# Performance work log

Hardware: AMD Instinct MI355X
Metric: run time of the kernel (lower is better)

## Reference

```python
import jax, jax.numpy as jnp
import numpy as np

C = 128          # hidden_channels
H = 8            # num_heads
D = C // H       # head dim = 16
OUT = 64         # out_channels
L = 2            # num_layers
NN = (30000, 60000, 6000)                 # poi, road, region node counts
NE = (200000, 300000, 200000, 100000)     # edges per edge type
ETS = ((0, 1), (1, 1), (1, 2), (2, 0))    # (src_type, dst_type) per edge type


def setup_inputs():
    key = jax.random.key(0)
    ks = iter(jax.random.split(key, 40))
    s = 1.0 / np.sqrt(C)
    sd = 1.0 / np.sqrt(D)
    inp = {}
    inp['x_poi'] = jax.random.normal(next(ks), (NN[0], C), jnp.float32)
    inp['x_road'] = jax.random.normal(next(ks), (NN[1], C), jnp.float32)
    inp['x_region'] = jax.random.normal(next(ks), (NN[2], C), jnp.float32)
    for et, (si, di) in enumerate(ETS):
        inp[f'e{et}_src'] = jax.random.randint(next(ks), (NE[et],), 0, NN[si], jnp.int32)
        inp[f'e{et}_dst'] = jax.random.randint(next(ks), (NE[et],), 0, NN[di], jnp.int32)
    # per-node-type input projection
    inp['lin_w'] = jax.random.normal(next(ks), (3, C, C), jnp.float32) * s
    inp['lin_b'] = jax.random.normal(next(ks), (3, C), jnp.float32) * 0.01
    # per-layer, per-node-type K/Q/V and output projections
    for nm in ('kw', 'qw', 'vw', 'aw'):
        inp[nm] = jax.random.normal(next(ks), (L, 3, C, C), jnp.float32) * s
    for nm in ('kb', 'qb', 'vb', 'ab'):
        inp[nm] = jax.random.normal(next(ks), (L, 3, C), jnp.float32) * 0.01
    # per-layer, per-edge-type relation matrices and priors
    inp['a_rel'] = jax.random.normal(next(ks), (L, 4, H, D, D), jnp.float32) * sd
    inp['m_rel'] = jax.random.normal(next(ks), (L, 4, H, D, D), jnp.float32) * sd
    inp['p_rel'] = jnp.ones((L, 4, H), jnp.float32)
    inp['skip'] = jnp.ones((L, 3), jnp.float32)
    inp['out_w'] = jax.random.normal(next(ks), (C, OUT), jnp.float32) * s
    inp['out_b'] = jnp.zeros((OUT,), jnp.float32)
    return inp


def _seg_softmax(alpha, dst, n):
    amax = jax.lax.stop_gradient(jax.ops.segment_max(alpha, dst, num_segments=n))
    ex = jnp.exp(alpha - amax[dst])
    den = jax.ops.segment_sum(ex, dst, num_segments=n)
    return ex / (den[dst] + 1e-16)


def _hgt_forward(xs, edges, lin_w, lin_b, kw, kb, qw, qb, vw, vb, aw, ab,
                 a_rel, m_rel, p_rel, skip, out_w, out_b):
    # per-node-type input linear + relu
    xs = [jax.nn.relu(xs[i] @ lin_w[i] + lin_b[i]) for i in range(3)]
    scale = 1.0 / np.sqrt(D)
    for l in range(L):
        k = [(xs[i] @ kw[l, i] + kb[l, i]).reshape(-1, H, D) for i in range(3)]
        q = [(xs[i] @ qw[l, i] + qb[l, i]).reshape(-1, H, D) for i in range(3)]
        v = [(xs[i] @ vw[l, i] + vb[l, i]).reshape(-1, H, D) for i in range(3)]
        agg = [jnp.zeros((NN[i], H, D), xs[i].dtype) for i in range(3)]
        for et, (si, di) in enumerate(ETS):
            src, dst = edges[et]
            n = NN[di]
            ke = jnp.einsum('ehd,hdf->ehf', k[si][src], a_rel[l, et])   # [E,H,D]
            alpha = jnp.einsum('ehd,ehd->eh', q[di][dst], ke) * p_rel[l, et] * scale
            alpha = _seg_softmax(alpha, dst, n)                          # [E,H]
            m = jnp.einsum('ehd,hdf->ehf', v[si][src], m_rel[l, et])    # [E,H,D]
            agg[di] = agg[di] + jax.ops.segment_sum(m * alpha[..., None], dst, num_segments=n)
        new_xs = []
        for i in range(3):
            o = jax.nn.gelu(agg[i].reshape(-1, C)) @ aw[l, i] + ab[l, i]
            beta = jax.nn.sigmoid(skip[l, i])
            o = beta * o + (1.0 - beta) * xs[i]
            new_xs.append(jax.nn.relu(o))  # HGT applies activation after each conv
        xs = new_xs
    return (xs[0] @ out_w + out_b, xs[1] @ out_w + out_b, xs[2] @ out_w + out_b)


def reference(x_poi, x_road, x_region,
              e0_src, e0_dst, e1_src, e1_dst, e2_src, e2_dst, e3_src, e3_dst,
              lin_w, lin_b, kw, kb, qw, qb, vw, vb, aw, ab,
              a_rel, m_rel, p_rel, skip, out_w, out_b):
    edges = ((e0_src, e0_dst), (e1_src, e1_dst), (e2_src, e2_dst), (e3_src, e3_dst))
    return _hgt_forward([x_poi, x_road, x_region], edges,
                        lin_w, lin_b, kw, kb, qw, qb, vw, vb, aw, ab,
                        a_rel, m_rel, p_rel, skip, out_w, out_b)
```

## Files before the change

### kernel.cpp

```cpp
#include <hip/hip_runtime.h>
#include <cstddef>
#include <cstdint>


typedef __attribute__((ext_vector_type(8))) short short8;
typedef __attribute__((ext_vector_type(4))) float floatx4;

__device__ __forceinline__ float gelu_fast(float x) {
    float u = 1.5957691216057308f * x * (1.0f + 0.044715f * x * x);
    return x / (1.0f + __expf(-u));
}

__device__ __forceinline__ unsigned short f2bf(float f) {
    unsigned u = __float_as_uint(f);
    u += 0x7fffu + ((u >> 16) & 1);
    return (unsigned short)(u >> 16);
}

__device__ __forceinline__ float bf2f(unsigned short h) {
    return __uint_as_float((unsigned)h << 16);
}

__device__ __forceinline__ void up8(uint4 u, float* f) {
    f[0] = __uint_as_float(u.x << 16); f[1] = __uint_as_float(u.x & 0xffff0000u);
    f[2] = __uint_as_float(u.y << 16); f[3] = __uint_as_float(u.y & 0xffff0000u);
    f[4] = __uint_as_float(u.z << 16); f[5] = __uint_as_float(u.z & 0xffff0000u);
    f[6] = __uint_as_float(u.w << 16); f[7] = __uint_as_float(u.w & 0xffff0000u);
}

__device__ __forceinline__ uint4 pk8(const float* f) {
    uint4 u;
    u.x = (unsigned)f2bf(f[0]) | ((unsigned)f2bf(f[1]) << 16);
    u.y = (unsigned)f2bf(f[2]) | ((unsigned)f2bf(f[3]) << 16);
    u.z = (unsigned)f2bf(f[4]) | ((unsigned)f2bf(f[5]) << 16);
    u.w = (unsigned)f2bf(f[6]) | ((unsigned)f2bf(f[7]) << 16);
    return u;
}

__global__ __launch_bounds__(256, 2) void gemm_proj_all(
    const unsigned short* __restrict__ xs_bf,
    const unsigned short* __restrict__ Wl,
    const float* __restrict__ bl,
    unsigned short* __restrict__ proj)
{
    const int    NN_[3]  = {30000, 60000, 6000};
    const int    NPAN[3] = {469, 938, 94};
    const int    OFFr[3] = {0, 30000, 90000};
    const int    WOFF[3] = {0, 49152, 131072};
    const int    BOFF[3] = {0, 384, 1024};
    const size_t POFF[3] = {0, 11520000u, 49920000u};
    const int    LDO[3]  = {384, 640, 384};

    int b = blockIdx.x, t, cp, rb;
    if (b < 590)      { t = 1; cp = b / 118; rb = b - cp * 118; }
    else if (b < 767) { int lb = b - 590; t = 0; cp = lb / 59; rb = lb - cp * 59; }
    else              { int lb = b - 767; t = 2; cp = lb / 12; rb = lb - cp * 12; }
    int p0 = rb * 8, p1 = p0 + 8;
    if (p1 > NPAN[t]) p1 = NPAN[t];

    const unsigned short* Abf = xs_bf + (size_t)OFFr[t] * 128;
    const unsigned short* Wt  = Wl + WOFF[t];
    const float* bias = bl + BOFF[t] + cp * 128;
    unsigned short* outbf = proj + POFF[t];
    const int ldo = LDO[t], Nrows = NN_[t];

    const int wave = threadIdx.x >> 6, lane = threadIdx.x & 63;
    const int quad = lane >> 4, l16 = lane & 15;

    short8 B[2][4][4];
    {
        const unsigned short* wb = Wt + (size_t)(cp * 128 + l16) * 128 + quad * 8;
        #pragma unroll
        for (int T = 0; T < 2; ++T)
            #pragma unroll
            for (int c = 0; c < 4; ++c)
                #pragma unroll
                for (int kc = 0; kc < 4; ++kc)
                    B[T][c][kc] = *(const short8*)(wb + (size_t)(T * 64 + c * 16) * 128 + kc * 32);
    }
    float4 bv[2][4];
    #pragma unroll
    for (int T = 0; T < 2; ++T)
        #pragma unroll
        for (int c = 0; c < 4; ++c)
            bv[T][c] = *(const float4*)(bias + T * 64 + c * 16 + quad * 4);

    short8 Acur[4];
    {
        int m = p0 * 64 + wave * 16 + l16; if (m >= Nrows) m = Nrows - 1;
        const unsigned short* ap = Abf + (size_t)m * 128 + quad * 8;
        #pragma unroll
        for (int kc = 0; kc < 4; ++kc) Acur[kc] = *(const short8*)(ap + kc * 32);
    }
    for (int p = p0; p < p1; ++p) {
        short8 Anx[4];
        {
            int m = (p + 1) * 64 + wave * 16 + l16; if (m >= Nrows) m = Nrows - 1;
            const unsigned short* ap = Abf + (size_t)m * 128 + quad * 8;
            #pragma unroll
            for (int kc = 0; kc < 4; ++kc) Anx[kc] = *(const short8*)(ap + kc * 32);
        }
        floatx4 acc[2][4];
        #pragma unroll
        for (int T = 0; T < 2; ++T)
            #pragma unroll
            for (int c = 0; c < 4; ++c) acc[T][c] = (floatx4){0.f, 0.f, 0.f, 0.f};
        #pragma unroll
        for (int kc = 0; kc < 4; ++kc)
            #pragma unroll
            for (int T = 0; T < 2; ++T)
                #pragma unroll
                for (int c = 0; c < 4; ++c)
                    acc[T][c] = __builtin_amdgcn_mfma_f32_16x16x32_bf16(B[T][c][kc], Acur[kc], acc[T][c], 0, 0, 0);
        int node = p * 64 + wave * 16 + l16;
        if (node < Nrows) {
            unsigned short* op = outbf + (size_t)node * ldo + cp * 128 + quad * 4;
            #pragma unroll
            for (int T = 0; T < 2; ++T)
                #pragma unroll
                for (int c = 0; c < 4; ++c) {
                    uint2 u;
                    u.x = (unsigned)f2bf(acc[T][c][0] + bv[T][c].x) |
                          ((unsigned)f2bf(acc[T][c][1] + bv[T][c].y) << 16);
                    u.y = (unsigned)f2bf(acc[T][c][2] + bv[T][c].z) |
                          ((unsigned)f2bf(acc[T][c][3] + bv[T][c].w) << 16);
                    *(uint2*)(op + T * 64 + c * 16) = u;
                }
        }
        #pragma unroll
        for (int kc = 0; kc < 4; ++kc) Acur[kc] = Anx[kc];
    }
}

template<bool AF32, bool GIN, bool SKIP>
__global__ __launch_bounds__(256, 2) void gemm_node(
    const void* __restrict__ a0v, const void* __restrict__ a1v, const void* __restrict__ a2v,
    const unsigned short* __restrict__ WtB, const float* __restrict__ biasB,
    const unsigned short* __restrict__ xoldB, const float* __restrict__ skipB,
    unsigned short* __restrict__ outB)
{
    const int TN[3]   = {30000, 60000, 6000};
    const int NPAN[3] = {469, 938, 94};
    const int TOFF[3] = {0, 30000, 90000};
    int b = blockIdx.x, t, rb;
    if (b < 118)      { t = 0; rb = b; }
    else if (b < 353) { t = 1; rb = b - 118; }
    else              { t = 2; rb = b - 353; }
    int p0 = rb * 4, p1 = p0 + 4;
    if (p1 > NPAN[t]) p1 = NPAN[t];
    int Nrows = TN[t];
    const void* av = (t == 0) ? a0v : (t == 1) ? a1v : a2v;
    const unsigned short* xold = xoldB + (size_t)TOFF[t] * 128;
    unsigned short* out = outB + (size_t)TOFF[t] * 128;

    const int wave = threadIdx.x >> 6, lane = threadIdx.x & 63;
    const int quad = lane >> 4, l16 = lane & 15;

    short8 B[8][4];
    {
        const unsigned short* wb = WtB + (size_t)t * 16384 + (size_t)l16 * 128 + quad * 8;
        #pragma unroll
        for (int c = 0; c < 8; ++c)
            #pragma unroll
            for (int kc = 0; kc < 4; ++kc)
                B[c][kc] = *(const short8*)(wb + (size_t)c * 2048 + kc * 32);
    }
    float beta = 0.f, omb = 0.f;
    if (SKIP) { beta = 1.0f / (1.0f + __expf(-skipB[t])); omb = 1.0f - beta; }

    short8 Acur[4];
    {
        int m = p0 * 64 + wave * 16 + l16; if (m >= Nrows) m = Nrows - 1;
        size_t base = (size_t)m * 128 + quad * 8;
        #pragma unroll
        for (int kc = 0; kc < 4; ++kc) {
            if (AF32) {
                const float* ap = (const float*)av + base;
                float4 f0 = *(const float4*)(ap + kc * 32);
                float4 f1 = *(const float4*)(ap + kc * 32 + 4);
                float af[8] = {f0.x, f0.y, f0.z, f0.w, f1.x, f1.y, f1.z, f1.w};
                short8 a;
                #pragma unroll
                for (int i = 0; i < 8; ++i) a[i] = (short)f2bf(af[i]);
                Acur[kc] = a;
            } else if (GIN) {
                const unsigned short* ap = (const unsigned short*)av + base;
                short8 a8 = *(const short8*)(ap + kc * 32);
                short8 a;
                #pragma unroll
                for (int i = 0; i < 8; ++i)
                    a[i] = (short)f2bf(gelu_fast(bf2f((unsigned short)a8[i])));
                Acur[kc] = a;
            } else {
                const unsigned short* ap = (const unsigned short*)av + base;
                Acur[kc] = *(const short8*)(ap + kc * 32);
            }
        }
    }
    for (int p = p0; p < p1; ++p) {
        float4 Fnx[4][2];
        short8 Snx[4];
        {
            int m = (p + 1) * 64 + wave * 16 + l16; if (m >= Nrows) m = Nrows - 1;
            size_t base = (size_t)m * 128 + quad * 8;
            #pragma unroll
            for (int kc = 0; kc < 4; ++kc) {
                if (AF32) {
                    const float* ap = (const float*)av + base;
                    Fnx[kc][0] = *(const float4*)(ap + kc * 32);
                    Fnx[kc][1] = *(const float4*)(ap + kc * 32 + 4);
                } else {
                    const unsigned short* ap = (const unsigned short*)av + base;
                    Snx[kc] = *(const short8*)(ap + kc * 32);
                }
            }
        }
        int node = p * 64 + wave * 16 + l16;
        int ncl = (node < Nrows) ? node : (Nrows - 1);
        uint2 xo[8];
        if (SKIP) {
            #pragma unroll
            for (int c = 0; c < 8; ++c)
                xo[c] = *(const uint2*)(xold + (size_t)ncl * 128 + c * 16 + quad * 4);
        }
        floatx4 acc[8];
        #pragma unroll
        for (int c = 0; c < 8; ++c) acc[c] = (floatx4){0.f, 0.f, 0.f, 0.f};
        #pragma unroll
        for (int kc = 0; kc < 4; ++kc)
            #pragma unroll
            for (int c = 0; c < 8; ++c)
                acc[c] = __builtin_amdgcn_mfma_f32_16x16x32_bf16(B[c][kc], Acur[kc], acc[c], 0, 0, 0);
        if (node < Nrows) {
            #pragma unroll
            for (int c = 0; c < 8; ++c) {
                int col0 = c * 16 + quad * 4;
                float4 bv = *(const float4*)(biasB + t * 128 + col0);
                float o0 = acc[c][0] + bv.x, o1 = acc[c][1] + bv.y;
                float o2 = acc[c][2] + bv.z, o3 = acc[c][3] + bv.w;
                if (SKIP) {
                    o0 = beta * o0 + omb * __uint_as_float(xo[c].x << 16);
                    o1 = beta * o1 + omb * __uint_as_float(xo[c].x & 0xffff0000u);
                    o2 = beta * o2 + omb * __uint_as_float(xo[c].y << 16);
                    o3 = beta * o3 + omb * __uint_as_float(xo[c].y & 0xffff0000u);
                }
                o0 = fmaxf(o0, 0.f); o1 = fmaxf(o1, 0.f);
                o2 = fmaxf(o2, 0.f); o3 = fmaxf(o3, 0.f);
                uint2 u;
                u.x = (unsigned)f2bf(o0) | ((unsigned)f2bf(o1) << 16);
                u.y = (unsigned)f2bf(o2) | ((unsigned)f2bf(o3) << 16);
                *(uint2*)(out + (size_t)node * 128 + col0) = u;
            }
        }
        #pragma unroll
        for (int kc = 0; kc < 4; ++kc) {
            if (AF32) {
                float af[8] = {Fnx[kc][0].x, Fnx[kc][0].y, Fnx[kc][0].z, Fnx[kc][0].w,
                               Fnx[kc][1].x, Fnx[kc][1].y, Fnx[kc][1].z, Fnx[kc][1].w};
                short8 a;
                #pragma unroll
                for (int i = 0; i < 8; ++i) a[i] = (short)f2bf(af[i]);
                Acur[kc] = a;
            } else if (GIN) {
                short8 a;
                #pragma unroll
                for (int i = 0; i < 8; ++i)
                    a[i] = (short)f2bf(gelu_fast(bf2f((unsigned short)Snx[kc][i])));
                Acur[kc] = a;
            } else {
                Acur[kc] = Snx[kc];
            }
        }
    }
}

__global__ __launch_bounds__(256, 3) void gemm_out(
    const unsigned short* __restrict__ Abf,
    const unsigned short* __restrict__ Wt,
    const float* __restrict__ bias,
    float* __restrict__ out, int Nrows)
{
    const int wave = threadIdx.x >> 6, lane = threadIdx.x & 63;
    const int quad = lane >> 4, l16 = lane & 15;
    int p0 = blockIdx.x * 4, p1 = p0 + 4;

    short8 B[4][4];
    {
        const unsigned short* wb = Wt + (size_t)l16 * 128 + quad * 8;
        #pragma unroll
        for (int c = 0; c < 4; ++c)
            #pragma unroll
            for (int kc = 0; kc < 4; ++kc)
                B[c][kc] = *(const short8*)(wb + (size_t)c * 2048 + kc * 32);
    }
    float4 bv[4];
    #pragma unroll
    for (int c = 0; c < 4; ++c) bv[c] = *(const float4*)(bias + c * 16 + quad * 4);

    short8 Acur[4];
    {
        int m = p0 * 64 + wave * 16 + l16; if (m >= Nrows) m = Nrows - 1;
        const unsigned short* ap = Abf + (size_t)m * 128 + quad * 8;
        #pragma unroll
        for (int kc = 0; kc < 4; ++kc) Acur[kc] = *(const short8*)(ap + kc * 32);
    }
    for (int p = p0; p < p1; ++p) {
        short8 Anx[4];
        {
            int m = (p + 1) * 64 + wave * 16 + l16; if (m >= Nrows) m = Nrows - 1;
            const unsigned short* ap = Abf + (size_t)m * 128 + quad * 8;
            #pragma unroll
            for (int kc = 0; kc < 4; ++kc) Anx[kc] = *(const short8*)(ap + kc * 32);
        }
        floatx4 acc[4];
        #pragma unroll
        for (int c = 0; c < 4; ++c) acc[c] = (floatx4){0.f, 0.f, 0.f, 0.f};
        #pragma unroll
        for (int kc = 0; kc < 4; ++kc)
            #pragma unroll
            for (int c = 0; c < 4; ++c)
                acc[c] = __builtin_amdgcn_mfma_f32_16x16x32_bf16(B[c][kc], Acur[kc], acc[c], 0, 0, 0);
        int node = p * 64 + wave * 16 + l16;
        if (node < Nrows) {
            #pragma unroll
            for (int c = 0; c < 4; ++c) {
                float4 o;
                o.x = acc[c][0] + bv[c].x; o.y = acc[c][1] + bv[c].y;
                o.z = acc[c][2] + bv[c].z; o.w = acc[c][3] + bv[c].w;
                *(float4*)(out + (size_t)node * 64 + c * 16 + quad * 4) = o;
            }
        }
        #pragma unroll
        for (int kc = 0; kc < 4; ++kc) Acur[kc] = Anx[kc];
    }
}

__global__ __launch_bounds__(128) void prep_all(
    const float* __restrict__ qw, const float* __restrict__ qb,
    const float* __restrict__ kw, const float* __restrict__ kb,
    const float* __restrict__ vw, const float* __restrict__ vb,
    const float* __restrict__ a_rel, const float* __restrict__ m_rel,
    const float* __restrict__ lin_w, const float* __restrict__ aw,
    const float* __restrict__ ow,
    unsigned short* __restrict__ Wpack, float* __restrict__ bpack,
    unsigned short* __restrict__ lwt, unsigned short* __restrict__ awt,
    unsigned short* __restrict__ owt)
{
    const int pre[3] = {0, 49152, 131072};
    const int preB[3] = {0, 384, 1024};
    int b = blockIdx.x;
    if (b < 768) {
        int n = threadIdx.x;
        int k = b & 127, r = b >> 7, t = r % 3, l = r / 3;
        unsigned short* Wp = Wpack + (size_t)l * 180224 + pre[t];
        Wp[(size_t)n * 128 + k] = f2bf(qw[(size_t)(l * 3 + t) * 16384 + (size_t)k * 128 + n]);
        if (k == 0) bpack[l * 1408 + preB[t] + n] = qb[(l * 3 + t) * 128 + n];
    } else if (b < 1792) {
        const int SIv[4] = {0, 1, 1, 2};
        const int SLOT[4] = {0, 0, 1, 0};
        int bb = b - 768;
        int hf = threadIdx.x, h = hf >> 4, f = hf & 15;
        int c = bb & 127, et = (bb >> 7) & 3, l = bb >> 9;
        int si = SIv[et];
        const float* kwp  = kw + (size_t)(l * 3 + si) * 16384;
        const float* vwp  = vw + (size_t)(l * 3 + si) * 16384;
        const float* kbp  = kb + (size_t)(l * 3 + si) * 128;
        const float* vbp  = vb + (size_t)(l * 3 + si) * 128;
        const float* arel = a_rel + (size_t)(l * 4 + et) * 2048;
        const float* mrel = m_rel + (size_t)(l * 4 + et) * 2048;
        float sk = 0.f, sv = 0.f;
        #pragma unroll
        for (int d = 0; d < 16; ++d) {
            float ar = arel[(h * 16 + d) * 16 + f];
            float mr = mrel[(h * 16 + d) * 16 + f];
            sk = fmaf(kwp[c * 128 + h * 16 + d], ar, sk);
            sv = fmaf(vwp[c * 128 + h * 16 + d], mr, sv);
        }
        int rowoff = 128 + 256 * SLOT[et];
        unsigned short* Wp = Wpack + (size_t)l * 180224 + pre[si];
        Wp[(size_t)(rowoff + hf) * 128 + c]       = f2bf(sk);
        Wp[(size_t)(rowoff + 128 + hf) * 128 + c] = f2bf(sv);
        if (c == 0) {
            float bk = 0.f, bvv = 0.f;
            #pragma unroll
            for (int d = 0; d < 16; ++d) {
                bk  = fmaf(kbp[h * 16 + d], arel[(h * 16 + d) * 16 + f], bk);
                bvv = fmaf(vbp[h * 16 + d], mrel[(h * 16 + d) * 16 + f], bvv);
            }
            float* bp = bpack + l * 1408 + preB[si];
            bp[rowoff + hf]       = bk;
            bp[rowoff + 128 + hf] = bvv;
        }
    } else if (b < 2944) {
        int bb = b - 1792;
        int n = threadIdx.x, k = bb & 127, mi = bb >> 7;
        const float* w; unsigned short* wt; int m;
        if (mi < 3) { w = lin_w; wt = lwt; m = mi; }
        else        { w = aw;    wt = awt; m = mi - 3; }
        wt[(size_t)m * 16384 + (size_t)n * 128 + k] =
            f2bf(w[(size_t)m * 16384 + (size_t)k * 128 + n]);
    } else {
        int k = b - 2944, n = threadIdx.x;
        if (n < 64) owt[(size_t)n * 128 + k] = f2bf(ow[(size_t)k * 64 + n]);
    }
}

__global__ __launch_bounds__(256) void hist_all(
    const int* __restrict__ d0, const int* __restrict__ d1,
    const int* __restrict__ d2, const int* __restrict__ d3,
    int* __restrict__ deg4)
{
    const int Ev[4] = {200000, 300000, 200000, 100000};
    int et = blockIdx.y;
    int e = blockIdx.x * 256 + threadIdx.x;
    if (e >= Ev[et]) return;
    const int* d = et == 0 ? d0 : et == 1 ? d1 : et == 2 ? d2 : d3;
    atomicAdd(&deg4[et * 60000 + d[e]], 1);
}

__global__ __launch_bounds__(256) void scan_tile_all(
    int* __restrict__ deg4,
    int* __restrict__ r0, int* __restrict__ r1, int* __restrict__ r2, int* __restrict__ r3,
    int* __restrict__ tsum4)
{
    const int Ndv[4] = {60000, 60000, 6000, 30000};
    __shared__ int ls[256];
    int et = blockIdx.y;
    int n = Ndv[et];
    int* deg = deg4 + et * 60000;
    int* rowptr = et == 0 ? r0 : et == 1 ? r1 : et == 2 ? r2 : r3;
    int b = blockIdx.x, tid = threadIdx.x;
    int base = b * 1024 + tid * 4;
    int v0 = 0, v1 = 0, v2 = 0, v3 = 0;
    if (base + 3 < n) {
        int4 t = *(const int4*)(deg + base);
        v0 = t.x; v1 = t.y; v2 = t.z; v3 = t.w;
        *(int4*)(deg + base) = make_int4(0, 0, 0, 0);
    } else {
        if (base + 0 < n) { v0 = deg[base + 0]; deg[base + 0] = 0; }
        if (base + 1 < n) { v1 = deg[base + 1]; deg[base + 1] = 0; }
        if (base + 2 < n) { v2 = deg[base + 2]; deg[base + 2] = 0; }
        if (base + 3 < n) { v3 = deg[base + 3]; deg[base + 3] = 0; }
    }
    int s = v0 + v1 + v2 + v3;
    ls[tid] = s;
    __syncthreads();
    #pragma unroll
    for (int off = 1; off < 256; off <<= 1) {
        int t = (tid >= off) ? ls[tid - off] : 0;
        __syncthreads();
        ls[tid] += t;
        __syncthreads();
    }
    int run = ls[tid] - s;
    int o0 = run; run += v0;
    int o1 = run; run += v1;
    int o2 = run; run += v2;
    int o3 = run;
    if (base + 3 < n) {
        *(int4*)(rowptr + base) = make_int4(o0, o1, o2, o3);
    } else {
        if (base + 0 < n) rowptr[base + 0] = o0;
        if (base + 1 < n) rowptr[base + 1] = o1;
        if (base + 2 < n) rowptr[base + 2] = o2;
    }
    if (tid == 255) tsum4[et * 64 + b] = ls[255];
}

__global__ __launch_bounds__(256) void scan_add_all(
    int* __restrict__ r0, int* __restrict__ r1, int* __restrict__ r2, int* __restrict__ r3,
    const int* __restrict__ tsum4)
{
    const int Ndv[4] = {60000, 60000, 6000, 30000};
    __shared__ int ts[64];
    int et = blockIdx.y;
    int n = Ndv[et];
    int* rowptr = et == 0 ? r0 : et == 1 ? r1 : et == 2 ? r2 : r3;
    int tid = threadIdx.x;
    if (tid < 64) ts[tid] = tsum4[et * 64 + tid];
    __syncthreads();
    int i = blockIdx.x * 256 + tid;
    int tile = i >> 10;
    int pre = 0;
    for (int j = 0; j < tile; ++j) pre += ts[j];
    if (i < n) rowptr[i] += pre;
    if (blockIdx.x == 0 && tid == 0) {
        int nt = (n + 1023) >> 10, tot = 0;
        for (int j = 0; j < nt; ++j) tot += ts[j];
        rowptr[n] = tot;
    }
}

__global__ __launch_bounds__(256) void fill_all(
    const int* __restrict__ s0, const int* __restrict__ d0,
    const int* __restrict__ s1, const int* __restrict__ d1,
    const int* __restrict__ s2, const int* __restrict__ d2,
    const int* __restrict__ s3, const int* __restrict__ d3,
    const int* __restrict__ r0, const int* __restrict__ r1,
    const int* __restrict__ r2, const int* __restrict__ r3,
    int* __restrict__ deg4,
    int* __restrict__ c0, int* __restrict__ c1, int* __restrict__ c2, int* __restrict__ c3)
{
    const int Ev[4] = {200000, 300000, 200000, 100000};
    int et = blockIdx.y;
    int e = blockIdx.x * 256 + threadIdx.x;
    if (e >= Ev[et]) return;
    const int* src = et == 0 ? s0 : et == 1 ? s1 : et == 2 ? s2 : s3;
    const int* dst = et == 0 ? d0 : et == 1 ? d1 : et == 2 ? d2 : d3;
    const int* rowptr = et == 0 ? r0 : et == 1 ? r1 : et == 2 ? r2 : r3;
    int* csr = et == 0 ? c0 : et == 1 ? c1 : et == 2 ? c2 : c3;
    int d = dst[e];
    int pos = atomicAdd(&deg4[et * 60000 + d], 1);
    csr[rowptr[d] + pos] = src[e];
}

__device__ __forceinline__ void attn_edge(
    uint4 k0, uint4 k1, uint4 v0, uint4 v1,
    const float* qf, float ph, float& m, float& l, float* o)
{
    float kf[16];
    up8(k0, kf); up8(k1, kf + 8);
    float a = 0.f;
    #pragma unroll
    for (int i = 0; i < 16; ++i) a = fmaf(qf[i], kf[i], a);
    a *= ph;
    float d = a - m;
    if (d > 8.f) {
        float sc = __expf(-d);
        l *= sc;
        #pragma unroll
        for (int i = 0; i < 16; ++i) o[i] *= sc;
        m = a; d = 0.f;
    }
    float w = __expf(d);
    l += w;
    float vf[16];
    up8(v0, vf); up8(v1, vf + 8);
    #pragma unroll
    for (int i = 0; i < 16; ++i) o[i] = fmaf(w, vf[i], o[i]);
}

__device__ __forceinline__ void attn_run(
    const int* __restrict__ csr, int beg, int end,
    const unsigned short* __restrict__ kbase, int ld,
    const float* qf, float ph, float& m, float& l, float* o)
{
    int n = end - beg;
    if (n <= 0) return;
    const uint4* pA = (const uint4*)(kbase + (size_t)csr[beg] * ld);
    uint4 A0 = pA[0], A1 = pA[1], A2 = pA[16], A3 = pA[17];
    uint4 B0 = A0, B1 = A1, B2 = A2, B3 = A3;
    if (n > 1) {
        const uint4* pB = (const uint4*)(kbase + (size_t)csr[beg + 1] * ld);
        B0 = pB[0]; B1 = pB[1]; B2 = pB[16]; B3 = pB[17];
    }
    int j = beg;
    for (; j + 3 < end; j += 2) {
        const uint4* pC = (const uint4*)(kbase + (size_t)csr[j + 2] * ld);
        const uint4* pD = (const uint4*)(kbase + (size_t)csr[j + 3] * ld);
        uint4 C0 = pC[0], C1 = pC[1], C2 = pC[16], C3 = pC[17];
        uint4 D0 = pD[0], D1 = pD[1], D2 = pD[16], D3 = pD[17];
        float kf0[16], kf1[16];
        up8(A0, kf0); up8(A1, kf0 + 8);
        up8(B0, kf1); up8(B1, kf1 + 8);
        float a0 = 0.f, a1 = 0.f;
        #pragma unroll
        for (int i = 0; i < 16; ++i) {
            a0 = fmaf(qf[i], kf0[i], a0);
            a1 = fmaf(qf[i], kf1[i], a1);
        }
        a0 *= ph; a1 *= ph;
        float hi = fmaxf(a0, a1);
        float d = hi - m;
        if (d > 8.f) {
            float sc = __expf(-d);
            l *= sc;
            #pragma unroll
            for (int i = 0; i < 16; ++i) o[i] *= sc;
            m = hi;
        }
        float w0 = __expf(a0 - m), w1 = __expf(a1 - m);
        l += w0 + w1;
        float vf0[16], vf1[16];
        up8(A2, vf0); up8(A3, vf0 + 8);
        up8(B2, vf1); up8(B3, vf1 + 8);
        #pragma unroll
        for (int i = 0; i < 16; ++i)
            o[i] = fmaf(w1, vf1[i], fmaf(w0, vf0[i], o[i]));
        A0 = C0; A1 = C1; A2 = C2; A3 = C3;
        B0 = D0; B1 = D1; B2 = D2; B3 = D3;
    }
    int rem = end - j;
    attn_edge(A0, A1, A2, A3, qf, ph, m, l, o);
    if (rem >= 2) attn_edge(B0, B1, B2, B3, qf, ph, m, l, o);
    if (rem == 3) {
        const uint4* pC = (const uint4*)(kbase + (size_t)csr[j + 2] * ld);
        attn_edge(pC[0], pC[1], pC[16], pC[17], qf, ph, m, l, o);
    }
}

__device__ __forceinline__ void merge_sm(float& m, float& l, float* o, int st)
{
    float mp = __shfl_xor(m, st);
    float lp = __shfl_xor(l, st);
    float mn = fmaxf(m, mp);
    float sc  = (l  > 0.f) ? __expf(m  - mn) : 0.f;
    float scp = (lp > 0.f) ? __expf(mp - mn) : 0.f;
    l = l * sc + lp * scp;
    #pragma unroll
    for (int i = 0; i < 16; ++i) {
        float op = __shfl_xor(o[i], st);
        o[i] = o[i] * sc + op * scp;
    }
    m = mn;
}

__global__ __launch_bounds__(256) void agg_all(
    const int* __restrict__ rp0, const int* __restrict__ cs0,
    const int* __restrict__ rp1, const int* __restrict__ cs1,
    const int* __restrict__ rp2, const int* __restrict__ cs2,
    const int* __restrict__ rp3, const int* __restrict__ cs3,
    const unsigned short* __restrict__ P0, const unsigned short* __restrict__ P1,
    const unsigned short* __restrict__ P2,
    const float* __restrict__ prl,
    unsigned short* __restrict__ num)
{
    int gb = blockIdx.x, tid = threadIdx.x;
    float qf[16], o[16], r[16];
    if (gb < 3750) {
        int t = gb * 256 + tid;
        int node = t >> 4, h = t & 7, half = (t >> 3) & 1;
        const uint4* qp = (const uint4*)(P1 + (size_t)node * 640 + h * 16);
        up8(qp[0], qf); up8(qp[1], qf + 8);
        const int* csr = half ? cs1 : cs0;
        const int* rp  = half ? rp1 : rp0;
        const unsigned short* kb = half ? (P1 + 128 + h * 16) : (P0 + 128 + h * 16);
        int ld = half ? 640 : 384;
        float ph = prl[(half ? 8 : 0) + h] * 0.25f;
        float m = -INFINITY, l = 0.f;
        #pragma unroll
        for (int i = 0; i < 16; ++i) o[i] = 0.f;
        attn_run(csr, rp[node], rp[node + 1], kb, ld, qf, ph, m, l, o);
        float inv = 1.f / (l + 1e-16f);
        #pragma unroll
        for (int i = 0; i < 16; ++i) r[i] = inv * o[i];
        #pragma unroll
        for (int i = 0; i < 16; ++i) r[i] += __shfl_xor(r[i], 8);
        if (half) return;
        uint4* np = (uint4*)(num + (size_t)(30000 + node) * 128 + h * 16);
        np[0] = pk8(r); np[1] = pk8(r + 8);
    } else if (gb < 4500) {
        int t = (gb - 3750) * 256 + tid;
        int node = t >> 5, h = t & 7, sub = (t >> 3) & 3;
        int beg0 = rp2[node], end0 = rp2[node + 1];
        int n = end0 - beg0;
        int beg = beg0 + ((n * sub) >> 2);
        int end = beg0 + ((n * (sub + 1)) >> 2);
        const uint4* qp = (const uint4*)(P2 + (size_t)node * 384 + h * 16);
        up8(qp[0], qf); up8(qp[1], qf + 8);
        float m = -INFINITY, l = 0.f;
        #pragma unroll
        for (int i = 0; i < 16; ++i) o[i] = 0.f;
        attn_run(cs2, beg, end, P1 + 384 + h * 16, 640,
                 qf, prl[16 + h] * 0.25f, m, l, o);
        merge_sm(m, l, o, 8);
        merge_sm(m, l, o, 16);
        if (sub) return;
        float inv = 1.f / (l + 1e-16f);
        #pragma unroll
        for (int i = 0; i < 16; ++i) r[i] = inv * o[i];
        uint4* np = (uint4*)(num + (size_t)(90000 + node) * 128 + h * 16);
        np[0] = pk8(r); np[1] = pk8(r + 8);
    } else {
        int t = (gb - 4500) * 256 + tid;
        if (t >= 240000) return;
        int node = t >> 3, h = t & 7;
        const uint4* qp = (const uint4*)(P0 + (size_t)node * 384 + h * 16);
        up8(qp[0], qf); up8(qp[1], qf + 8);
        float m = -INFINITY, l = 0.f;
        #pragma unroll
        for (int i = 0; i < 16; ++i) o[i] = 0.f;
        attn_run(cs3, rp3[node], rp3[node + 1], P2 + 128 + h * 16, 384,
                 qf, prl[24 + h] * 0.25f, m, l, o);
        float inv = 1.f / (l + 1e-16f);
        #pragma unroll
        for (int i = 0; i < 16; ++i) r[i] = inv * o[i];
        uint4* np = (uint4*)(num + (size_t)node * 128 + h * 16);
        np[0] = pk8(r); np[1] = pk8(r + 8);
    }
}

extern "C" void kernel_launch(void* const* d_in, const int* in_sizes, int n_in,
                              void* d_out, int out_size, void* d_ws, size_t ws_size,
                              hipStream_t stream)
{
    (void)in_sizes; (void)n_in; (void)out_size; (void)ws_size;

    const float* xin[3] = {(const float*)d_in[0], (const float*)d_in[1], (const float*)d_in[2]};
    const int* esrc[4] = {(const int*)d_in[3], (const int*)d_in[5], (const int*)d_in[7], (const int*)d_in[9]};
    const int* edst[4] = {(const int*)d_in[4], (const int*)d_in[6], (const int*)d_in[8], (const int*)d_in[10]};
    const float* lin_w = (const float*)d_in[11];
    const float* lin_b = (const float*)d_in[12];
    const float* kw = (const float*)d_in[13];
    const float* qw = (const float*)d_in[14];
    const float* vw = (const float*)d_in[15];
    const float* aw = (const float*)d_in[16];
    const float* kb = (const float*)d_in[17];
    const float* qb = (const float*)d_in[18];
    const float* vb = (const float*)d_in[19];
    const float* ab = (const float*)d_in[20];
    const float* a_rel = (const float*)d_in[21];
    const float* m_rel = (const float*)d_in[22];
    const float* p_rel = (const float*)d_in[23];
    const float* skip  = (const float*)d_in[24];
    const float* out_w = (const float*)d_in[25];
    const float* out_b = (const float*)d_in[26];

    float* ws = (float*)d_ws;
    unsigned short* num   = (unsigned short*)ws;
    unsigned short* xs_bf = (unsigned short*)(ws + 6144000);
    unsigned short* proj  = (unsigned short*)(ws + 12288000);
    unsigned short* Wpack = (unsigned short*)(ws + 38400000);
    unsigned short* lwt   = (unsigned short*)(ws + 38580224);
    unsigned short* awt   = (unsigned short*)(ws + 38604800);
    unsigned short* owt   = (unsigned short*)(ws + 38653952);
    float*          bpack = ws + 38658048;
    int*            deg4  = (int*)(ws + 38660864);
    int*            tsum4 = (int*)(ws + 38900864);
    int* rp[4];
    rp[0] = (int*)(ws + 38901120);
    rp[1] = (int*)(ws + 38961128);
    rp[2] = (int*)(ws + 39021136);
    rp[3] = (int*)(ws + 39027144);
    int* cs[4];
    cs[0] = (int*)(ws + 39057152);
    cs[1] = (int*)(ws + 39257152);
    cs[2] = (int*)(ws + 39557152);
    cs[3] = (int*)(ws + 39757152);

    unsigned short* P[3];
    P[0] = proj;
    P[1] = proj + (size_t)30000 * 384;
    P[2] = proj + (size_t)30000 * 384 + (size_t)60000 * 640;

    dim3 blk(256);

    hipMemsetAsync(deg4, 0, 960000, stream);
    hist_all<<<dim3(1172, 4), blk, 0, stream>>>(edst[0], edst[1], edst[2], edst[3], deg4);
    scan_tile_all<<<dim3(59, 4), blk, 0, stream>>>(deg4, rp[0], rp[1], rp[2], rp[3], tsum4);
    scan_add_all<<<dim3(235, 4), blk, 0, stream>>>(rp[0], rp[1], rp[2], rp[3], tsum4);
    fill_all<<<dim3(1172, 4), blk, 0, stream>>>(
        esrc[0], edst[0], esrc[1], edst[1], esrc[2], edst[2], esrc[3], edst[3],
        rp[0], rp[1], rp[2], rp[3], deg4, cs[0], cs[1], cs[2], cs[3]);

    prep_all<<<dim3(3072), dim3(128), 0, stream>>>(
        qw, qb, kw, kb, vw, vb, a_rel, m_rel, lin_w, aw, out_w,
        Wpack, bpack, lwt, awt, owt);

    gemm_node<true, false, false><<<dim3(377), blk, 0, stream>>>(
        xin[0], xin[1], xin[2], lwt, lin_b, nullptr, nullptr, xs_bf);

    for (int l = 0; l < 2; ++l) {
        gemm_proj_all<<<dim3(803), blk, 0, stream>>>(
            xs_bf, Wpack + (size_t)l * 180224, bpack + l * 1408, proj);

        agg_all<<<dim3(5438), blk, 0, stream>>>(
            rp[0], cs[0], rp[1], cs[1], rp[2], cs[2], rp[3], cs[3],
            P[0], P[1], P[2], p_rel + (size_t)l * 32, num);

        gemm_node<false, true, true><<<dim3(377), blk, 0, stream>>>(
            num, num + (size_t)30000 * 128, num + (size_t)90000 * 128,
            awt + (size_t)l * 3 * 16384, ab + (size_t)l * 3 * 128,
            xs_bf, skip + l * 3, xs_bf);
    }

    gemm_out<<<dim3(375), blk, 0, stream>>>(
        xs_bf, owt, out_b, (float*)d_out, 96000);
}
```

Before: 567.5 us.

## Fuse histogram with weight prep and CSR fill with input projection GEMM

Merges the degree-histogram kernel with the weight-packing prep kernel into one launch, and merges the CSR fill kernel with the input-projection GEMM, dispatching by block index. This cuts two kernel launches and lets the independent graph-building and dense work run concurrently on different blocks. The new input GEMM computes all 128 output columns per wave with 4 panels per block and a ReLU epilogue. It adds register pressure, through launch_bounds(256,2) and 32 B fragments held per lane, and mixes heterogeneous blocks in one grid.

Measured after the change: 555.2 us. 1.02x faster.

```diff
diff --git a/kernel.cpp b/kernel.cpp
--- a/kernel.cpp
+++ b/kernel.cpp
@@ -335,7 +335,10 @@
     }
 }
 
-__global__ __launch_bounds__(128) void prep_all(
+__global__ __launch_bounds__(256) void hist_prep(
+    const int* __restrict__ d0, const int* __restrict__ d1,
+    const int* __restrict__ d2, const int* __restrict__ d3,
+    int* __restrict__ deg4,
     const float* __restrict__ qw, const float* __restrict__ qb,
     const float* __restrict__ kw, const float* __restrict__ kb,
     const float* __restrict__ vw, const float* __restrict__ vb,
@@ -346,20 +349,31 @@
     unsigned short* __restrict__ lwt, unsigned short* __restrict__ awt,
     unsigned short* __restrict__ owt)
 {
+    int b = blockIdx.x;
+    if (b < 4688) {
+        const int Ev[4] = {200000, 300000, 200000, 100000};
+        int et = b / 1172, bx = b - et * 1172;
+        int e = bx * 256 + threadIdx.x;
+        if (e >= Ev[et]) return;
+        const int* d = et == 0 ? d0 : et == 1 ? d1 : et == 2 ? d2 : d3;
+        atomicAdd(&deg4[et * 60000 + d[e]], 1);
+        return;
+    }
     const int pre[3] = {0, 49152, 131072};
     const int preB[3] = {0, 384, 1024};
-    int b = blockIdx.x;
-    if (b < 768) {
-        int n = threadIdx.x;
-        int k = b & 127, r = b >> 7, t = r % 3, l = r / 3;
+    int unit = (b - 4688) * 2 + (threadIdx.x >> 7);
+    int tid = threadIdx.x & 127;
+    if (unit < 768) {
+        int n = tid;
+        int k = unit & 127, r = unit >> 7, t = r % 3, l = r / 3;
         unsigned short* Wp = Wpack + (size_t)l * 180224 + pre[t];
         Wp[(size_t)n * 128 + k] = f2bf(qw[(size_t)(l * 3 + t) * 16384 + (size_t)k * 128 + n]);
         if (k == 0) bpack[l * 1408 + preB[t] + n] = qb[(l * 3 + t) * 128 + n];
-    } else if (b < 1792) {
+    } else if (unit < 1792) {
         const int SIv[4] = {0, 1, 1, 2};
         const int SLOT[4] = {0, 0, 1, 0};
-        int bb = b - 768;
-        int hf = threadIdx.x, h = hf >> 4, f = hf & 15;
+        int bb = unit - 768;
+        int hf = tid, h = hf >> 4, f = hf & 15;
         int c = bb & 127, et = (bb >> 7) & 3, l = bb >> 9;
         int si = SIv[et];
         const float* kwp  = kw + (size_t)(l * 3 + si) * 16384;
@@ -391,31 +405,18 @@
             bp[rowoff + hf]       = bk;
             bp[rowoff + 128 + hf] = bvv;
         }
-    } else if (b < 2944) {
-        int bb = b - 1792;
-        int n = threadIdx.x, k = bb & 127, mi = bb >> 7;
+    } else if (unit < 2944) {
+        int bb = unit - 1792;
+        int n = tid, k = bb & 127, mi = bb >> 7;
         const float* w; unsigned short* wt; int m;
         if (mi < 3) { w = lin_w; wt = lwt; m = mi; }
         else        { w = aw;    wt = awt; m = mi - 3; }
         wt[(size_t)m * 16384 + (size_t)n * 128 + k] =
             f2bf(w[(size_t)m * 16384 + (size_t)k * 128 + n]);
     } else {
-        int k = b - 2944, n = threadIdx.x;
+        int k = unit - 2944, n = tid;
         if (n < 64) owt[(size_t)n * 128 + k] = f2bf(ow[(size_t)k * 64 + n]);
     }
-}
-
-__global__ __launch_bounds__(256) void hist_all(
-    const int* __restrict__ d0, const int* __restrict__ d1,
-    const int* __restrict__ d2, const int* __restrict__ d3,
-    int* __restrict__ deg4)
-{
-    const int Ev[4] = {200000, 300000, 200000, 100000};
-    int et = blockIdx.y;
-    int e = blockIdx.x * 256 + threadIdx.x;
-    if (e >= Ev[et]) return;
-    const int* d = et == 0 ? d0 : et == 1 ? d1 : et == 2 ? d2 : d3;
-    atomicAdd(&deg4[et * 60000 + d[e]], 1);
 }
 
 __global__ __launch_bounds__(256) void scan_tile_all(
@@ -491,7 +492,7 @@
     }
 }
 
-__global__ __launch_bounds__(256) void fill_all(
+__global__ __launch_bounds__(256, 2) void fill_nodein(
     const int* __restrict__ s0, const int* __restrict__ d0,
     const int* __restrict__ s1, const int* __restrict__ d1,
     const int* __restrict__ s2, const int* __restrict__ d2,
@@ -499,19 +500,114 @@
     const int* __restrict__ r0, const int* __restrict__ r1,
     const int* __restrict__ r2, const int* __restrict__ r3,
     int* __restrict__ deg4,
-    int* __restrict__ c0, int* __restrict__ c1, int* __restrict__ c2, int* __restrict__ c3)
-{
-    const int Ev[4] = {200000, 300000, 200000, 100000};
-    int et = blockIdx.y;
-    int e = blockIdx.x * 256 + threadIdx.x;
-    if (e >= Ev[et]) return;
-    const int* src = et == 0 ? s0 : et == 1 ? s1 : et == 2 ? s2 : s3;
-    const int* dst = et == 0 ? d0 : et == 1 ? d1 : et == 2 ? d2 : d3;
-    const int* rowptr = et == 0 ? r0 : et == 1 ? r1 : et == 2 ? r2 : r3;
-    int* csr = et == 0 ? c0 : et == 1 ? c1 : et == 2 ? c2 : c3;
-    int d = dst[e];
-    int pos = atomicAdd(&deg4[et * 60000 + d], 1);
-    csr[rowptr[d] + pos] = src[e];
+    int* __restrict__ c0, int* __restrict__ c1, int* __restrict__ c2, int* __restrict__ c3,
+    const float* __restrict__ x0, const float* __restrict__ x1,
+    const float* __restrict__ x2,
+    const unsigned short* __restrict__ lwt, const float* __restrict__ lin_b,
+    unsigned short* __restrict__ xs_bf)
+{
+    int b = blockIdx.x;
+    if (b < 4688) {
+        const int Ev[4] = {200000, 300000, 200000, 100000};
+        int et = b / 1172, bx = b - et * 1172;
+        int e = bx * 256 + threadIdx.x;
+        if (e >= Ev[et]) return;
+        const int* src = et == 0 ? s0 : et == 1 ? s1 : et == 2 ? s2 : s3;
+        const int* dst = et == 0 ? d0 : et == 1 ? d1 : et == 2 ? d2 : d3;
+        const int* rowptr = et == 0 ? r0 : et == 1 ? r1 : et == 2 ? r2 : r3;
+        int* csr = et == 0 ? c0 : et == 1 ? c1 : et == 2 ? c2 : c3;
+        int dd = dst[e];
+        int pos = atomicAdd(&deg4[et * 60000 + dd], 1);
+        csr[rowptr[dd] + pos] = src[e];
+        return;
+    }
+    const int TN[3]   = {30000, 60000, 6000};
+    const int NPAN[3] = {469, 938, 94};
+    const int TOFF[3] = {0, 30000, 90000};
+    int nb = b - 4688, t, rb;
+    if (nb < 118)      { t = 0; rb = nb; }
+    else if (nb < 353) { t = 1; rb = nb - 118; }
+    else               { t = 2; rb = nb - 353; }
+    int p0 = rb * 4, p1 = p0 + 4;
+    if (p1 > NPAN[t]) p1 = NPAN[t];
+    int Nrows = TN[t];
+    const float* av = (t == 0) ? x0 : (t == 1) ? x1 : x2;
+    unsigned short* out = xs_bf + (size_t)TOFF[t] * 128;
+
+    const int wave = threadIdx.x >> 6, lane = threadIdx.x & 63;
+    const int quad = lane >> 4, l16 = lane & 15;
+
+    short8 B[8][4];
+    {
+        const unsigned short* wb = lwt + (size_t)t * 16384 + (size_t)l16 * 128 + quad * 8;
+        #pragma unroll
+        for (int c = 0; c < 8; ++c)
+            #pragma unroll
+            for (int kc = 0; kc < 4; ++kc)
+                B[c][kc] = *(const short8*)(wb + (size_t)c * 2048 + kc * 32);
+    }
+    short8 Acur[4];
+    {
+        int m = p0 * 64 + wave * 16 + l16; if (m >= Nrows) m = Nrows - 1;
+        size_t base = (size_t)m * 128 + quad * 8;
+        #pragma unroll
+        for (int kc = 0; kc < 4; ++kc) {
+            const float* ap = av + base;
+            float4 f0 = *(const float4*)(ap + kc * 32);
+            float4 f1 = *(const float4*)(ap + kc * 32 + 4);
+            float af[8] = {f0.x, f0.y, f0.z, f0.w, f1.x, f1.y, f1.z, f1.w};
+            short8 a;
+            #pragma unroll
+            for (int i = 0; i < 8; ++i) a[i] = (short)f2bf(af[i]);
+            Acur[kc] = a;
+        }
+    }
+    for (int p = p0; p < p1; ++p) {
+        float4 Fnx[4][2];
+        {
+            int m = (p + 1) * 64 + wave * 16 + l16; if (m >= Nrows) m = Nrows - 1;
+            size_t base = (size_t)m * 128 + quad * 8;
+            #pragma unroll
+            for (int kc = 0; kc < 4; ++kc) {
+                const float* ap = av + base;
+                Fnx[kc][0] = *(const float4*)(ap + kc * 32);
+                Fnx[kc][1] = *(const float4*)(ap + kc * 32 + 4);
+            }
+        }
+        floatx4 acc[8];
+        #pragma unroll
+        for (int c = 0; c < 8; ++c) acc[c] = (floatx4){0.f, 0.f, 0.f, 0.f};
+        #pragma unroll
+        for (int kc = 0; kc < 4; ++kc)
+            #pragma unroll
+            for (int c = 0; c < 8; ++c)
+                acc[c] = __builtin_amdgcn_mfma_f32_16x16x32_bf16(B[c][kc], Acur[kc], acc[c], 0, 0, 0);
+        int node = p * 64 + wave * 16 + l16;
+        if (node < Nrows) {
+            #pragma unroll
+            for (int c = 0; c < 8; ++c) {
+                int col0 = c * 16 + quad * 4;
+                float4 bv = *(const float4*)(lin_b + t * 128 + col0);
+                float o0 = fmaxf(acc[c][0] + bv.x, 0.f);
+                float o1 = fmaxf(acc[c][1] + bv.y, 0.f);
+                float o2 = fmaxf(acc[c][2] + bv.z, 0.f);
+                float o3 = fmaxf(acc[c][3] + bv.w, 0.f);
+                uint2 u;
+                u.x = (unsigned)f2bf(o0) | ((unsigned)f2bf(o1) << 16);
+                u.y = (unsigned)f2bf(o2) | ((unsigned)f2bf(o3) << 16);
+                *(uint2*)(out + (size_t)node * 128 + col0) = u;
+            }
+        }
+        #pragma unroll
+        for (int kc = 0; kc < 4; ++kc) {
+            float af[8] = {Fnx[kc][0].x, Fnx[kc][0].y, Fnx[kc][0].z, Fnx[kc][0].w,
+                           Fnx[kc][1].x, Fnx[kc][1].y, Fnx[kc][1].z, Fnx[kc][1].w};
+            short8 a;
+            #pragma unroll
+            for (int i = 0; i < 8; ++i) a[i] = (short)f2bf(af[i]);
+            Acur[kc] = a;
+        }
+    }
 }
 
 __device__ __forceinline__ void attn_edge(
@@ -746,19 +842,17 @@
     dim3 blk(256);
 
     hipMemsetAsync(deg4, 0, 960000, stream);
-    hist_all<<<dim3(1172, 4), blk, 0, stream>>>(edst[0], edst[1], edst[2], edst[3], deg4);
+    hist_prep<<<dim3(6224), blk, 0, stream>>>(
+        edst[0], edst[1], edst[2], edst[3], deg4,
+        qw, qb, kw, kb, vw, vb, a_rel, m_rel, lin_w, aw, out_w,
+        Wpack, bpack, lwt, awt, owt);
     scan_tile_all<<<dim3(59, 4), blk, 0, stream>>>(deg4, rp[0], rp[1], rp[2], rp[3], tsum4);
     scan_add_all<<<dim3(235, 4), blk, 0, stream>>>(rp[0], rp[1], rp[2], rp[3], tsum4);
-    fill_all<<<dim3(1172, 4), blk, 0, stream>>>(
+
+    fill_nodein<<<dim3(5065), blk, 0, stream>>>(
         esrc[0], edst[0], esrc[1], edst[1], esrc[2], edst[2], esrc[3], edst[3],
-        rp[0], rp[1], rp[2], rp[3], deg4, cs[0], cs[1], cs[2], cs[3]);
-
-    prep_all<<<dim3(3072), dim3(128), 0, stream>>>(
-        qw, qb, kw, kb, vw, vb, a_rel, m_rel, lin_w, aw, out_w,
-        Wpack, bpack, lwt, awt, owt);
-
-    gemm_node<true, false, false><<<dim3(377), blk, 0, stream>>>(
-        xin[0], xin[1], xin[2], lwt, lin_b, nullptr, nullptr, xs_bf);
+        rp[0], rp[1], rp[2], rp[3], deg4, cs[0], cs[1], cs[2], cs[3],
+        xin[0], xin[1], xin[2], lwt, lin_b, xs_bf);
 
     for (int l = 0; l < 2; ++l) {
         gemm_proj_all<<<dim3(803), blk, 0, stream>>>(
```
